# Kernel optimization log

Measured on AMD Instinct MI355X. Metric: run time of the kernel, lower is better.

The kernel has to match this reference:

```python
import jax, jax.numpy as jnp
import numpy as np

B, S, H, C = 32, 1024, 768, 3
EPS = 1e-5
SCALE = 1.0 / np.sqrt(H)  # both nsa_norm_fact and _norm_fact equal 1/sqrt(H)


def _ln2d(x):
    # LayerNorm over last two dims [S, H] jointly, no learned affine (freshly-built torch LN)
    mu = jnp.mean(x, axis=(1, 2), keepdims=True)
    var = jnp.mean(jnp.square(x - mu), axis=(1, 2), keepdims=True)
    return (x - mu) * jax.lax.rsqrt(var + EPS)


def setup_inputs() -> dict:
    key = jax.random.key(0)
    ks = jax.random.split(key, 8)
    std = 1.0 / np.sqrt(H)
    return {
        "tokens": jax.random.normal(ks[0], (B, S, H), jnp.float32),
        "Wq": jax.random.normal(ks[1], (H, H), jnp.float32) * std,
        "bq": jnp.zeros((H,), jnp.float32),
        "Wk": jax.random.normal(ks[2], (H, H), jnp.float32) * std,
        "bk": jnp.zeros((H,), jnp.float32),
        "Wv": jax.random.normal(ks[3], (H, H), jnp.float32) * std,
        "bv": jnp.zeros((H,), jnp.float32),
        "W_sgsa": jax.random.normal(ks[4], (1, H), jnp.float32) * std,
        "b_sgsa": jnp.zeros((1,), jnp.float32),
        "W_fnn": jax.random.normal(ks[5], (C, 2 * H), jnp.float32) / np.sqrt(2 * H),
        "b_fnn": jnp.zeros((C,), jnp.float32),
    }


def reference(tokens, Wq, bq, Wk, bk, Wv, bv, W_sgsa, b_sgsa, W_fnn, b_fnn):
    # --- token self-attention (standard QK^T softmax V) ---
    Q = tokens @ Wq.T + bq
    K = tokens @ Wk.T + bk
    V = tokens @ Wv.T + bv
    attn = jax.nn.softmax(jnp.einsum("bsd,btd->bst", Q, K) * SCALE, axis=-1)
    out = jnp.einsum("bst,btd->bsd", attn, V)  # [B,S,H]

    out_ln = _ln2d(out)

    # --- channel attention (transposed Q^T K) using the SAME q/k/v weights ---
    Qn = out_ln @ Wq.T + bq
    Kn = out_ln @ Wk.T + bk
    Vn = out_ln @ Wv.T + bv
    attn_n = jax.nn.softmax(jnp.einsum("bsd,bse->bde", Qn, Kn) * SCALE, axis=-1)  # [B,H,H]
    out_n = jnp.einsum("bsd,bde->bse", Vn, attn_n)  # V_N @ attention_N

    out_n = tokens + out_n
    out_ln2 = _ln2d(out_n)

    # --- SGSA gate, mean/max pool, classifier ---
    gate = out_ln2 @ W_sgsa.T + b_sgsa          # [B,S,1]
    sgsa = gate * out_ln2                        # [B,S,H]
    pooled = jnp.concatenate([jnp.mean(sgsa, axis=1), jnp.max(sgsa, axis=1)], axis=1)  # [B,2H]
    return pooled @ W_fnn.T + b_fnn              # [B,C]
```

## Files before the change

kernel.cpp:

```cpp
#include <hip/hip_runtime.h>
#include <hip/hip_bf16.h>

typedef __hip_bfloat16 bf16;
typedef __attribute__((ext_vector_type(8))) short short8;
typedef __attribute__((ext_vector_type(4))) float f32x4;

#define DEVI __device__ __forceinline__

static constexpr int Bb = 32;
static constexpr int Ss = 1024;
static constexpr int Hh = 768;
static constexpr float LNEPS = 1e-5f;

DEVI void async16(const bf16* g, bf16* l) {
    __builtin_amdgcn_global_load_lds(
        (const __attribute__((address_space(1))) unsigned int*)g,
        (__attribute__((address_space(3))) unsigned int*)l,
        16, 0, 0);
}

DEVI unsigned fkey(float f) {
    unsigned u = __float_as_uint(f);
    return (u & 0x80000000u) ? ~u : (u | 0x80000000u);
}
DEVI float funkey(unsigned k) {
    return (k & 0x80000000u) ? __uint_as_float(k ^ 0x80000000u) : __uint_as_float(~k);
}

#define EPI_BF16_BIAS  0
#define EPI_BF16_SCALE 1
#define EPI_F32        2
#define EPI_F32_RES    3

template<int EPI>
__global__ __launch_bounds__(256)
void gemm_bt(const bf16* __restrict__ A, const bf16* __restrict__ Bt,
             void* __restrict__ Cv, const float* __restrict__ bias,
             const float* __restrict__ res,
             int M, int N, int K,
             long sA, long sB, long sC, long sRes, float scale)
{
    __shared__ bf16 As[128 * 32];
    __shared__ bf16 Bs[128 * 32];

    const int z = blockIdx.z;
    A  += (long)z * sA;
    Bt += (long)z * sB;

    const int n0  = blockIdx.x * 128;
    const int m0  = blockIdx.y * 128;
    const int tid = threadIdx.x;
    const int lane = tid & 63;
    const int w  = tid >> 6;
    const int wr = w >> 1, wc = w & 1;

    f32x4 acc[4][4];
    #pragma unroll
    for (int i = 0; i < 4; ++i)
        #pragma unroll
        for (int j = 0; j < 4; ++j) acc[i][j] = (f32x4){0.f, 0.f, 0.f, 0.f};

    const int c0 = tid,        r0 = c0 >> 2, kc0 = (c0 & 3) * 8;
    const int c1 = tid + 256,  r1 = c1 >> 2, kc1 = (c1 & 3) * 8;

    const int fr_row = lane & 15;
    const int fr_k   = (lane >> 4) * 8;

    const int nK = K >> 5;
    for (int kt = 0; kt < nK; ++kt) {
        const int k0 = kt << 5;
        async16(&A [(long)(m0 + r0) * K + k0 + kc0], &As[c0 * 8]);
        async16(&A [(long)(m0 + r1) * K + k0 + kc1], &As[c1 * 8]);
        async16(&Bt[(long)(n0 + r0) * K + k0 + kc0], &Bs[c0 * 8]);
        async16(&Bt[(long)(n0 + r1) * K + k0 + kc1], &Bs[c1 * 8]);
        __syncthreads();

        short8 af[4], bfr[4];
        #pragma unroll
        for (int i = 0; i < 4; ++i) {
            af [i] = *(const short8*)&As[(wr * 64 + i * 16 + fr_row) * 32 + fr_k];
            bfr[i] = *(const short8*)&Bs[(wc * 64 + i * 16 + fr_row) * 32 + fr_k];
        }
        #pragma unroll
        for (int mi = 0; mi < 4; ++mi)
            #pragma unroll
            for (int ni = 0; ni < 4; ++ni)
                acc[mi][ni] = __builtin_amdgcn_mfma_f32_16x16x32_bf16(
                    af[mi], bfr[ni], acc[mi][ni], 0, 0, 0);
        __syncthreads();
    }

    #pragma unroll
    for (int mi = 0; mi < 4; ++mi) {
        #pragma unroll
        for (int ni = 0; ni < 4; ++ni) {
            const int col = n0 + wc * 64 + ni * 16 + (lane & 15);
            #pragma unroll
            for (int r = 0; r < 4; ++r) {
                const int row = m0 + wr * 64 + mi * 16 + (lane >> 4) * 4 + r;
                float v = acc[mi][ni][r];
                const long ci = (long)z * sC + (long)row * N + col;
                if constexpr (EPI == EPI_BF16_BIAS) {
                    ((bf16*)Cv)[ci] = __float2bfloat16(v + bias[col]);
                } else if constexpr (EPI == EPI_BF16_SCALE) {
                    ((bf16*)Cv)[ci] = __float2bfloat16(v * scale);
                } else if constexpr (EPI == EPI_F32) {
                    ((float*)Cv)[ci] = v;
                } else {
                    ((float*)Cv)[ci] = v + res[(long)z * sRes + (long)row * N + col];
                }
            }
        }
    }
}


__global__ void cvt_bf16(const float* __restrict__ x, bf16* __restrict__ y, long n4) {
    long i = (long)blockIdx.x * 256 + threadIdx.x;
    if (i >= n4) return;
    float4 v = *(const float4*)&x[i * 4];
    union { bf16 h[4]; unsigned long long u; } pk;
    pk.h[0] = __float2bfloat16(v.x); pk.h[1] = __float2bfloat16(v.y);
    pk.h[2] = __float2bfloat16(v.z); pk.h[3] = __float2bfloat16(v.w);
    *(unsigned long long*)&y[i * 4] = pk.u;
}

__global__ void transpose_bf16(const bf16* __restrict__ in, bf16* __restrict__ out,
                               int R, int C, long sIn, long sOut)
{
    __shared__ bf16 tile[32][33];
    const int z = blockIdx.z;
    in  += (long)z * sIn;
    out += (long)z * sOut;
    const int cb = blockIdx.x * 32, rb = blockIdx.y * 32;
    const int tx = threadIdx.x & 31, ty = threadIdx.x >> 5;
    #pragma unroll
    for (int i = 0; i < 4; ++i) {
        int r = ty + i * 8;
        tile[r][tx] = in[(long)(rb + r) * C + cb + tx];
    }
    __syncthreads();
    #pragma unroll
    for (int i = 0; i < 4; ++i) {
        int r = ty + i * 8;
        out[(long)(cb + r) * R + rb + tx] = tile[tx][r];
    }
}

template<int CNT>
__global__ void softmax_rows(bf16* __restrict__ P) {
    const int W = CNT * 256;
    bf16* p = P + (long)blockIdx.x * W;
    const int tid = threadIdx.x;
    float v[CNT];
    float mx = -3.0e38f;
    #pragma unroll
    for (int i = 0; i < CNT; ++i) {
        v[i] = __bfloat162float(p[tid + i * 256]);
        mx = fmaxf(mx, v[i]);
    }
    #pragma unroll
    for (int o = 32; o; o >>= 1) mx = fmaxf(mx, __shfl_xor(mx, o));
    __shared__ float sm[4], ss[4];
    if ((tid & 63) == 0) sm[tid >> 6] = mx;
    __syncthreads();
    mx = fmaxf(fmaxf(sm[0], sm[1]), fmaxf(sm[2], sm[3]));
    float s = 0.f;
    #pragma unroll
    for (int i = 0; i < CNT; ++i) { v[i] = __expf(v[i] - mx); s += v[i]; }
    #pragma unroll
    for (int o = 32; o; o >>= 1) s += __shfl_xor(s, o);
    if ((tid & 63) == 0) ss[tid >> 6] = s;
    __syncthreads();
    s = ss[0] + ss[1] + ss[2] + ss[3];
    const float inv = 1.0f / s;
    #pragma unroll
    for (int i = 0; i < CNT; ++i) p[tid + i * 256] = __float2bfloat16(v[i] * inv);
}

__global__ void ln_stats(const float* __restrict__ x, float* __restrict__ stats, int perB) {
    const int b = blockIdx.y;
    const float* xb = x + (long)b * perB;
    const int tid = threadIdx.x;
    const long base = (long)blockIdx.x * 4096;
    float s1 = 0.f, s2 = 0.f;
    #pragma unroll
    for (int i = 0; i < 4; ++i) {
        float4 v = *(const float4*)&xb[base + i * 1024 + tid * 4];
        s1 += v.x + v.y + v.z + v.w;
        s2 += v.x * v.x + v.y * v.y + v.z * v.z + v.w * v.w;
    }
    #pragma unroll
    for (int o = 32; o; o >>= 1) { s1 += __shfl_xor(s1, o); s2 += __shfl_xor(s2, o); }
    __shared__ float r1[4], r2[4];
    if ((tid & 63) == 0) { r1[tid >> 6] = s1; r2[tid >> 6] = s2; }
    __syncthreads();
    if (tid == 0) {
        atomicAdd(&stats[b * 2],     r1[0] + r1[1] + r1[2] + r1[3]);
        atomicAdd(&stats[b * 2 + 1], r2[0] + r2[1] + r2[2] + r2[3]);
    }
}

DEVI void ln_params(const float* stats, int b, float n, float& mu, float& rs) {
    mu = stats[b * 2] / n;
    float var = stats[b * 2 + 1] / n - mu * mu;
    rs = rsqrtf(fmaxf(var, 0.f) + LNEPS);
}

__global__ void ln_apply(const float* __restrict__ x, const float* __restrict__ stats,
                         bf16* __restrict__ y, int perB)
{
    const long i4 = ((long)blockIdx.x * 256 + threadIdx.x) * 4;
    const int b = (int)(i4 / perB);
    float mu, rs; ln_params(stats, b, (float)perB, mu, rs);
    float4 v = *(const float4*)&x[i4];
    union { bf16 h[4]; unsigned long long u; } pk;
    pk.h[0] = __float2bfloat16((v.x - mu) * rs);
    pk.h[1] = __float2bfloat16((v.y - mu) * rs);
    pk.h[2] = __float2bfloat16((v.z - mu) * rs);
    pk.h[3] = __float2bfloat16((v.w - mu) * rs);
    *(unsigned long long*)&y[i4] = pk.u;
}

__global__ void gate_kernel(const float* __restrict__ xn, const float* __restrict__ Wsg,
                            const float* __restrict__ bsg, const float* __restrict__ stats2,
                            const float* __restrict__ sumW, float* __restrict__ gate)
{
    const long row = blockIdx.x;
    const int b = (int)(row >> 10);
    const float* xr = xn + row * Hh;
    const int tid = threadIdx.x;
    float d = 0.f;
    #pragma unroll
    for (int j = 0; j < 3; ++j) d += xr[tid + j * 256] * Wsg[tid + j * 256];
    #pragma unroll
    for (int o = 32; o; o >>= 1) d += __shfl_xor(d, o);
    __shared__ float sr[4];
    if ((tid & 63) == 0) sr[tid >> 6] = d;
    __syncthreads();
    if (tid == 0) {
        float mu, rs; ln_params(stats2, b, (float)(Ss * Hh), mu, rs);
        gate[row] = rs * ((sr[0] + sr[1] + sr[2] + sr[3]) - mu * sumW[0]) + bsg[0];
    }
}

__global__ void pool_kernel(const float* __restrict__ xn, const float* __restrict__ gate,
                            const float* __restrict__ stats2, float* __restrict__ psum,
                            unsigned* __restrict__ pmax)
{
    const int b = blockIdx.y;
    const int s0 = blockIdx.x * 128;
    const int tid = threadIdx.x;
    float mu, rs; ln_params(stats2, b, (float)(Ss * Hh), mu, rs);
    const float* xb = xn + (long)b * (Ss * Hh);
    float sum[3] = {0.f, 0.f, 0.f};
    float mx[3]  = {-3e38f, -3e38f, -3e38f};
    for (int s = s0; s < s0 + 128; ++s) {
        float g = gate[(b << 10) + s];
        #pragma unroll
        for (int j = 0; j < 3; ++j) {
            float v = g * (xb[(long)s * Hh + tid + j * 256] - mu) * rs;
            sum[j] += v;
            mx[j] = fmaxf(mx[j], v);
        }
    }
    #pragma unroll
    for (int j = 0; j < 3; ++j) {
        atomicAdd(&psum[b * Hh + tid + j * 256], sum[j]);
        atomicMax(&pmax[b * Hh + tid + j * 256], fkey(mx[j]));
    }
}

__global__ void classifier(const float* __restrict__ psum, const unsigned* __restrict__ pmax,
                           const float* __restrict__ Wf, const float* __restrict__ bfn,
                           float* __restrict__ out)
{
    const int b = blockIdx.x, tid = threadIdx.x;
    float a0 = 0.f, a1 = 0.f, a2 = 0.f;
    for (int h = tid; h < Hh; h += 256) {
        float mean = psum[b * Hh + h] * (1.f / (float)Ss);
        float mxv  = funkey(pmax[b * Hh + h]);
        a0 += mean * Wf[0 * 1536 + h] + mxv * Wf[0 * 1536 + Hh + h];
        a1 += mean * Wf[1 * 1536 + h] + mxv * Wf[1 * 1536 + Hh + h];
        a2 += mean * Wf[2 * 1536 + h] + mxv * Wf[2 * 1536 + Hh + h];
    }
    #pragma unroll
    for (int o = 32; o; o >>= 1) {
        a0 += __shfl_xor(a0, o); a1 += __shfl_xor(a1, o); a2 += __shfl_xor(a2, o);
    }
    __shared__ float r[3][4];
    if ((tid & 63) == 0) { int w = tid >> 6; r[0][w] = a0; r[1][w] = a1; r[2][w] = a2; }
    __syncthreads();
    if (tid < 3) out[b * 3 + tid] = r[tid][0] + r[tid][1] + r[tid][2] + r[tid][3] + bfn[tid];
}

__global__ void init_ws(float* stats1, float* stats2, float* psum, unsigned* pmax,
                        float* sumW, const float* Wsg)
{
    const int tid = threadIdx.x;
    if (tid < 64) { stats1[tid] = 0.f; stats2[tid] = 0.f; }
    for (int i = tid; i < Bb * Hh; i += 256) { psum[i] = 0.f; pmax[i] = 0u; }
    float s = 0.f;
    for (int i = tid; i < Hh; i += 256) s += Wsg[i];
    #pragma unroll
    for (int o = 32; o; o >>= 1) s += __shfl_xor(s, o);
    __shared__ float sr[4];
    if ((tid & 63) == 0) sr[tid >> 6] = s;
    __syncthreads();
    if (tid == 0) sumW[0] = sr[0] + sr[1] + sr[2] + sr[3];
}

__global__ void sentinel_kernel(float* out, int n) {
    int i = blockIdx.x * 256 + threadIdx.x;
    if (i < n) out[i] = -12345.0f;
}


extern "C" void kernel_launch(void* const* d_in, const int* in_sizes, int n_in,
                              void* d_out, int out_size, void* d_ws, size_t ws_size,
                              hipStream_t stream)
{
    const float* tokens = (const float*)d_in[0];
    const float* Wq  = (const float*)d_in[1];
    const float* bq  = (const float*)d_in[2];
    const float* Wk  = (const float*)d_in[3];
    const float* bk  = (const float*)d_in[4];
    const float* Wv  = (const float*)d_in[5];
    const float* bv  = (const float*)d_in[6];
    const float* Wsg = (const float*)d_in[7];
    const float* bsg = (const float*)d_in[8];
    const float* Wf  = (const float*)d_in[9];
    const float* bfn = (const float*)d_in[10];
    float* out = (float*)d_out;

    const long BSH = (long)Bb * Ss * Hh;
    const long HH  = (long)Hh * Hh;
    const long BSS = (long)Bb * Ss * Ss;
    const long SH  = (long)Ss * Hh;
    const float SCALE = 1.0f / sqrtf((float)Hh);

    char* w = (char*)d_ws;
    size_t off = 0;
    auto alloc = [&](size_t bytes) -> void* {
        off = (off + 255) & ~(size_t)255;
        void* p = w + off;
        off += bytes;
        return p;
    };
    bf16*  wqB = (bf16*)alloc(HH * 2);
    bf16*  wkB = (bf16*)alloc(HH * 2);
    bf16*  wvB = (bf16*)alloc(HH * 2);
    bf16*  X0  = (bf16*)alloc(BSH * 2);
    bf16*  X1  = (bf16*)alloc(BSH * 2);
    bf16*  X2  = (bf16*)alloc(BSH * 2);
    bf16*  X4  = (bf16*)alloc(BSH * 2);
    bf16*  SP  = (bf16*)alloc(BSS * 2);
    float* stats1 = (float*)alloc(256);
    float* stats2 = (float*)alloc(256);
    float* sumW   = (float*)alloc(256);
    float* psum   = (float*)alloc((size_t)Bb * Hh * 4);
    unsigned* pmax = (unsigned*)alloc((size_t)Bb * Hh * 4);
    float* gate   = (float*)alloc((size_t)Bb * Ss * 4);
    const size_t need = off;
    (void)in_sizes; (void)n_in;

    if (ws_size < need) {
        sentinel_kernel<<<1, 256, 0, stream>>>(out, out_size);
        return;
    }

    bf16*  tokB = X0;
    bf16*  Qb   = X1;
    bf16*  Kb   = X2;
    bf16*  Vb   = SP;
    bf16*  VT   = X4;
    float* OF   = (float*)X1;

    init_ws<<<1, 256, 0, stream>>>(stats1, stats2, psum, pmax, sumW, Wsg);

    cvt_bf16<<<(int)(BSH / 1024), 256, 0, stream>>>(tokens, tokB, BSH / 4);
    cvt_bf16<<<(int)(HH / 1024), 256, 0, stream>>>(Wq, wqB, HH / 4);
    cvt_bf16<<<(int)(HH / 1024), 256, 0, stream>>>(Wk, wkB, HH / 4);
    cvt_bf16<<<(int)(HH / 1024), 256, 0, stream>>>(Wv, wvB, HH / 4);

    {
        dim3 g(Hh / 128, (Bb * Ss) / 128, 1);
        gemm_bt<EPI_BF16_BIAS><<<g, 256, 0, stream>>>(tokB, wqB, Qb, bq, nullptr,
            Bb * Ss, Hh, Hh, 0, 0, 0, 0, 1.f);
        gemm_bt<EPI_BF16_BIAS><<<g, 256, 0, stream>>>(tokB, wkB, Kb, bk, nullptr,
            Bb * Ss, Hh, Hh, 0, 0, 0, 0, 1.f);
        gemm_bt<EPI_BF16_BIAS><<<g, 256, 0, stream>>>(tokB, wvB, Vb, bv, nullptr,
            Bb * Ss, Hh, Hh, 0, 0, 0, 0, 1.f);
    }
    transpose_bf16<<<dim3(Hh / 32, Ss / 32, Bb), 256, 0, stream>>>(Vb, VT, Ss, Hh, SH, SH);

    gemm_bt<EPI_BF16_SCALE><<<dim3(Ss / 128, Ss / 128, Bb), 256, 0, stream>>>(
        Qb, Kb, SP, nullptr, nullptr, Ss, Ss, Hh, SH, SH, (long)Ss * Ss, 0, SCALE);
    softmax_rows<4><<<Bb * Ss, 256, 0, stream>>>(SP);

    gemm_bt<EPI_F32><<<dim3(Hh / 128, Ss / 128, Bb), 256, 0, stream>>>(
        SP, VT, OF, nullptr, nullptr, Ss, Hh, Ss, (long)Ss * Ss, SH, SH, 0, 1.f);

    ln_stats<<<dim3(192, Bb), 256, 0, stream>>>(OF, stats1, Ss * Hh);
    ln_apply<<<(int)(BSH / 1024), 256, 0, stream>>>(OF, stats1, tokB, Ss * Hh);

    bf16* Qn = X1; bf16* Kn = X2; bf16* Vn = SP;
    {
        dim3 g(Hh / 128, (Bb * Ss) / 128, 1);
        gemm_bt<EPI_BF16_BIAS><<<g, 256, 0, stream>>>(tokB, wqB, Qn, bq, nullptr,
            Bb * Ss, Hh, Hh, 0, 0, 0, 0, 1.f);
        gemm_bt<EPI_BF16_BIAS><<<g, 256, 0, stream>>>(tokB, wkB, Kn, bk, nullptr,
            Bb * Ss, Hh, Hh, 0, 0, 0, 0, 1.f);
        gemm_bt<EPI_BF16_BIAS><<<g, 256, 0, stream>>>(tokB, wvB, Vn, bv, nullptr,
            Bb * Ss, Hh, Hh, 0, 0, 0, 0, 1.f);
    }

    bf16* QnT = X4;
    bf16* KnT = X1;
    transpose_bf16<<<dim3(Hh / 32, Ss / 32, Bb), 256, 0, stream>>>(Qn, QnT, Ss, Hh, SH, SH);
    transpose_bf16<<<dim3(Hh / 32, Ss / 32, Bb), 256, 0, stream>>>(Kn, KnT, Ss, Hh, SH, SH);

    bf16* Sn = X2;
    gemm_bt<EPI_BF16_SCALE><<<dim3(Hh / 128, Hh / 128, Bb), 256, 0, stream>>>(
        QnT, KnT, Sn, nullptr, nullptr, Hh, Hh, Ss, SH, SH, HH, 0, SCALE);
    softmax_rows<3><<<Bb * Hh, 256, 0, stream>>>(Sn);

    bf16* PnT = X4;
    transpose_bf16<<<dim3(Hh / 32, Hh / 32, Bb), 256, 0, stream>>>(Sn, PnT, Hh, Hh, HH, HH);

    float* OF2 = (float*)X1;
    gemm_bt<EPI_F32_RES><<<dim3(Hh / 128, Ss / 128, Bb), 256, 0, stream>>>(
        Vn, PnT, OF2, nullptr, tokens, Ss, Hh, Hh, SH, HH, SH, SH, 1.f);

    ln_stats<<<dim3(192, Bb), 256, 0, stream>>>(OF2, stats2, Ss * Hh);
    gate_kernel<<<Bb * Ss, 256, 0, stream>>>(OF2, Wsg, bsg, stats2, sumW, gate);
    pool_kernel<<<dim3(Ss / 128, Bb), 256, 0, stream>>>(OF2, gate, stats2, psum, pmax);
    classifier<<<Bb, 256, 0, stream>>>(psum, pmax, Wf, bfn, out);
}
```

Baseline: 1.360 ms.

## Swizzle GEMM LDS layout, remap workgroups, and vectorize transpose and softmax

Result: faster. 1.206 ms (-11.3%).

```diff
diff --git a/kernel.cpp b/kernel.cpp
--- a/kernel.cpp
+++ b/kernel.cpp
@@ -2,6 +2,7 @@
 #include <hip/hip_bf16.h>
 
 typedef __hip_bfloat16 bf16;
+typedef unsigned short u16;
 typedef __attribute__((ext_vector_type(8))) short short8;
 typedef __attribute__((ext_vector_type(4))) float f32x4;
 
@@ -25,6 +26,10 @@
 }
 DEVI float funkey(unsigned k) {
     return (k & 0x80000000u) ? __uint_as_float(k ^ 0x80000000u) : __uint_as_float(~k);
+}
+DEVI u16 f2bu(float x) {
+    bf16 h = __float2bfloat16(x);
+    union { bf16 b; u16 u; } c; c.b = h; return c.u;
 }
 
 #define EPI_BF16_BIAS  0
@@ -43,12 +48,26 @@
     __shared__ bf16 As[128 * 32];
     __shared__ bf16 Bs[128 * 32];
 
-    const int z = blockIdx.z;
+    const int nx = gridDim.x, ny = gridDim.y;
+    int bx, by, z;
+    {
+        const int nxy = nx * ny;
+        const int nwg = nxy * gridDim.z;
+        int t = blockIdx.x + nx * (blockIdx.y + ny * blockIdx.z);
+        if ((nwg & 7) == 0) {
+            const int q = nwg >> 3;
+            t = (t & 7) * q + (t >> 3);
+        }
+        z  = t / nxy;
+        const int r2 = t - z * nxy;
+        by = r2 / nx;
+        bx = r2 - by * nx;
+    }
     A  += (long)z * sA;
     Bt += (long)z * sB;
 
-    const int n0  = blockIdx.x * 128;
-    const int m0  = blockIdx.y * 128;
+    const int n0  = bx * 128;
+    const int m0  = by * 128;
     const int tid = threadIdx.x;
     const int lane = tid & 63;
     const int w  = tid >> 6;
@@ -60,11 +79,11 @@
         #pragma unroll
         for (int j = 0; j < 4; ++j) acc[i][j] = (f32x4){0.f, 0.f, 0.f, 0.f};
 
-    const int c0 = tid,        r0 = c0 >> 2, kc0 = (c0 & 3) * 8;
-    const int c1 = tid + 256,  r1 = c1 >> 2, kc1 = (c1 & 3) * 8;
+    const int c0 = tid,        r0 = c0 >> 2, kc0 = (((c0 & 3) ^ ((r0 >> 1) & 3)) * 8);
+    const int c1 = tid + 256,  r1 = c1 >> 2, kc1 = (((c1 & 3) ^ ((r1 >> 1) & 3)) * 8);
 
     const int fr_row = lane & 15;
-    const int fr_k   = (lane >> 4) * 8;
+    const int kk = (((lane >> 4) ^ ((fr_row >> 1) & 3)) * 8);
 
     const int nK = K >> 5;
     for (int kt = 0; kt < nK; ++kt) {
@@ -78,8 +97,8 @@
         short8 af[4], bfr[4];
         #pragma unroll
         for (int i = 0; i < 4; ++i) {
-            af [i] = *(const short8*)&As[(wr * 64 + i * 16 + fr_row) * 32 + fr_k];
-            bfr[i] = *(const short8*)&Bs[(wc * 64 + i * 16 + fr_row) * 32 + fr_k];
+            af [i] = *(const short8*)&As[(wr * 64 + i * 16 + fr_row) * 32 + kk];
+            bfr[i] = *(const short8*)&Bs[(wc * 64 + i * 16 + fr_row) * 32 + kk];
         }
         #pragma unroll
         for (int mi = 0; mi < 4; ++mi)
@@ -125,39 +144,49 @@
     *(unsigned long long*)&y[i * 4] = pk.u;
 }
 
-__global__ void transpose_bf16(const bf16* __restrict__ in, bf16* __restrict__ out,
+__global__ void transpose_bf16(const bf16* __restrict__ in_, bf16* __restrict__ out_,
                                int R, int C, long sIn, long sOut)
 {
-    __shared__ bf16 tile[32][33];
-    const int z = blockIdx.z;
-    in  += (long)z * sIn;
-    out += (long)z * sOut;
-    const int cb = blockIdx.x * 32, rb = blockIdx.y * 32;
-    const int tx = threadIdx.x & 31, ty = threadIdx.x >> 5;
+    __shared__ u16 tile[64][70];
+    const u16* in  = (const u16*)in_  + (long)blockIdx.z * sIn;
+    u16*       out = (u16*)out_       + (long)blockIdx.z * sOut;
+    const int cb = blockIdx.x * 64, rb = blockIdx.y * 64;
+    const int lx = threadIdx.x & 15, ly = threadIdx.x >> 4;
     #pragma unroll
     for (int i = 0; i < 4; ++i) {
-        int r = ty + i * 8;
-        tile[r][tx] = in[(long)(rb + r) * C + cb + tx];
+        const int r = ly + i * 16;
+        ushort4 v = *(const ushort4*)&in[(long)(rb + r) * C + cb + lx * 4];
+        *(unsigned*)&tile[r][lx * 4]     = (unsigned)v.x | ((unsigned)v.y << 16);
+        *(unsigned*)&tile[r][lx * 4 + 2] = (unsigned)v.z | ((unsigned)v.w << 16);
     }
     __syncthreads();
     #pragma unroll
     for (int i = 0; i < 4; ++i) {
-        int r = ty + i * 8;
-        out[(long)(cb + r) * R + rb + tx] = tile[tx][r];
-    }
-}
-
-template<int CNT>
+        const int ro = ly + i * 16;
+        ushort4 o;
+        o.x = tile[lx * 4 + 0][ro];
+        o.y = tile[lx * 4 + 1][ro];
+        o.z = tile[lx * 4 + 2][ro];
+        o.w = tile[lx * 4 + 3][ro];
+        *(ushort4*)&out[(long)(cb + ro) * R + rb + lx * 4] = o;
+    }
+}
+
+template<int W>
 __global__ void softmax_rows(bf16* __restrict__ P) {
-    const int W = CNT * 256;
-    bf16* p = P + (long)blockIdx.x * W;
-    const int tid = threadIdx.x;
-    float v[CNT];
+    constexpr int NV = W / 4;
+    u16* p = (u16*)(P + (long)blockIdx.x * W);
+    const int tid = threadIdx.x;
+    const bool act = tid < NV;
+    float v[4];
     float mx = -3.0e38f;
-    #pragma unroll
-    for (int i = 0; i < CNT; ++i) {
-        v[i] = __bfloat162float(p[tid + i * 256]);
-        mx = fmaxf(mx, v[i]);
+    if (act) {
+        ushort4 u4 = ((const ushort4*)p)[tid];
+        v[0] = __uint_as_float((unsigned)u4.x << 16);
+        v[1] = __uint_as_float((unsigned)u4.y << 16);
+        v[2] = __uint_as_float((unsigned)u4.z << 16);
+        v[3] = __uint_as_float((unsigned)u4.w << 16);
+        mx = fmaxf(fmaxf(v[0], v[1]), fmaxf(v[2], v[3]));
     }
     #pragma unroll
     for (int o = 32; o; o >>= 1) mx = fmaxf(mx, __shfl_xor(mx, o));
@@ -166,16 +195,24 @@
     __syncthreads();
     mx = fmaxf(fmaxf(sm[0], sm[1]), fmaxf(sm[2], sm[3]));
     float s = 0.f;
-    #pragma unroll
-    for (int i = 0; i < CNT; ++i) { v[i] = __expf(v[i] - mx); s += v[i]; }
+    if (act) {
+        #pragma unroll
+        for (int j = 0; j < 4; ++j) { v[j] = __expf(v[j] - mx); s += v[j]; }
+    }
     #pragma unroll
     for (int o = 32; o; o >>= 1) s += __shfl_xor(s, o);
     if ((tid & 63) == 0) ss[tid >> 6] = s;
     __syncthreads();
     s = ss[0] + ss[1] + ss[2] + ss[3];
     const float inv = 1.0f / s;
-    #pragma unroll
-    for (int i = 0; i < CNT; ++i) p[tid + i * 256] = __float2bfloat16(v[i] * inv);
+    if (act) {
+        ushort4 o4;
+        o4.x = f2bu(v[0] * inv);
+        o4.y = f2bu(v[1] * inv);
+        o4.z = f2bu(v[2] * inv);
+        o4.w = f2bu(v[3] * inv);
+        ((ushort4*)p)[tid] = o4;
+    }
 }
 
 __global__ void ln_stats(const float* __restrict__ x, float* __restrict__ stats, int perB) {
@@ -392,11 +429,11 @@
         gemm_bt<EPI_BF16_BIAS><<<g, 256, 0, stream>>>(tokB, wvB, Vb, bv, nullptr,
             Bb * Ss, Hh, Hh, 0, 0, 0, 0, 1.f);
     }
-    transpose_bf16<<<dim3(Hh / 32, Ss / 32, Bb), 256, 0, stream>>>(Vb, VT, Ss, Hh, SH, SH);
+    transpose_bf16<<<dim3(Hh / 64, Ss / 64, Bb), 256, 0, stream>>>(Vb, VT, Ss, Hh, SH, SH);
 
     gemm_bt<EPI_BF16_SCALE><<<dim3(Ss / 128, Ss / 128, Bb), 256, 0, stream>>>(
         Qb, Kb, SP, nullptr, nullptr, Ss, Ss, Hh, SH, SH, (long)Ss * Ss, 0, SCALE);
-    softmax_rows<4><<<Bb * Ss, 256, 0, stream>>>(SP);
+    softmax_rows<1024><<<Bb * Ss, 256, 0, stream>>>(SP);
 
     gemm_bt<EPI_F32><<<dim3(Hh / 128, Ss / 128, Bb), 256, 0, stream>>>(
         SP, VT, OF, nullptr, nullptr, Ss, Hh, Ss, (long)Ss * Ss, SH, SH, 0, 1.f);
@@ -417,16 +454,16 @@
 
     bf16* QnT = X4;
     bf16* KnT = X1;
-    transpose_bf16<<<dim3(Hh / 32, Ss / 32, Bb), 256, 0, stream>>>(Qn, QnT, Ss, Hh, SH, SH);
-    transpose_bf16<<<dim3(Hh / 32, Ss / 32, Bb), 256, 0, stream>>>(Kn, KnT, Ss, Hh, SH, SH);
+    transpose_bf16<<<dim3(Hh / 64, Ss / 64, Bb), 256, 0, stream>>>(Qn, QnT, Ss, Hh, SH, SH);
+    transpose_bf16<<<dim3(Hh / 64, Ss / 64, Bb), 256, 0, stream>>>(Kn, KnT, Ss, Hh, SH, SH);
 
     bf16* Sn = X2;
     gemm_bt<EPI_BF16_SCALE><<<dim3(Hh / 128, Hh / 128, Bb), 256, 0, stream>>>(
         QnT, KnT, Sn, nullptr, nullptr, Hh, Hh, Ss, SH, SH, HH, 0, SCALE);
-    softmax_rows<3><<<Bb * Hh, 256, 0, stream>>>(Sn);
+    softmax_rows<768><<<Bb * Hh, 256, 0, stream>>>(Sn);
 
     bf16* PnT = X4;
-    transpose_bf16<<<dim3(Hh / 32, Hh / 32, Bb), 256, 0, stream>>>(Sn, PnT, Hh, Hh, HH, HH);
+    transpose_bf16<<<dim3(Hh / 64, Hh / 64, Bb), 256, 0, stream>>>(Sn, PnT, Hh, Hh, HH, HH);
 
     float* OF2 = (float*)X1;
     gemm_bt<EPI_F32_RES><<<dim3(Hh / 128, Ss / 128, Bb), 256, 0, stream>>>(
```
